# Optimization experiments

Hardware: AMD Instinct MI355X
Metric: run time of the kernel (lower is better)

Reference implementation:

```python
import jax, jax.numpy as jnp
import numpy as np

B, S, D, H = 2, 2048, 1024, 16
HD = D // H  # per-head dim = 64


def setup_inputs() -> dict:
    key = jax.random.key(0)
    ks = jax.random.split(key, 9)
    s = 0.02
    return {
        "h": jax.random.normal(ks[0], (B, S, D), jnp.float32),
        "Wq": jax.random.normal(ks[1], (D, D), jnp.float32) * s,
        "bq": jax.random.normal(ks[2], (D,), jnp.float32) * s,
        "Wk": jax.random.normal(ks[3], (D, D), jnp.float32) * s,
        "bk": jax.random.normal(ks[4], (D,), jnp.float32) * s,
        "Wv": jax.random.normal(ks[5], (D, D), jnp.float32) * s,
        "bv": jax.random.normal(ks[6], (D,), jnp.float32) * s,
        "Wo": jax.random.normal(ks[7], (D, D), jnp.float32) * s,
        "bo": jax.random.normal(ks[8], (D,), jnp.float32) * s,
    }


def reference(h, Wq, bq, Wk, bk, Wv, bv, Wo, bo):
    b, s, d = h.shape
    # Linear projections (torch Linear: x @ W.T + b), split heads -> [B,H,S,HD]
    def split_heads(x):
        return x.reshape(b, s, H, HD).transpose(0, 2, 1, 3)

    q = split_heads(h @ Wq.T + bq)
    k = split_heads(h @ Wk.T + bk)
    v = split_heads(h @ Wv.T + bv)

    # scaled scores [B,H,S,S]
    qk = jnp.einsum("bhqd,bhkd->bhqk", q, k) / np.sqrt(HD).astype(np.float32)
    # causal mask: strictly upper triangle -> -inf
    causal = jnp.triu(jnp.ones((s, s), dtype=bool), k=1)
    qk = jnp.where(causal[None, None], -jnp.inf, qk)

    probs = jax.nn.softmax(qk, axis=-1)
    o = jnp.einsum("bhqk,bhkd->bhqd", probs, v)
    o = o.transpose(0, 2, 1, 3).reshape(b, s, d)
    return o @ Wo.T + bo
```

## Files before the change

### kernel.cpp

```cpp
#include <hip/hip_runtime.h>
#include <stdint.h>

typedef __bf16 bf16;
typedef __bf16 bf16x4_t __attribute__((ext_vector_type(4)));
typedef __bf16 bf16x8_t __attribute__((ext_vector_type(8)));
typedef float f32x4 __attribute__((ext_vector_type(4)));

static constexpr int NB = 2, SS = 2048, DD = 1024, NH = 16, HD = 64;

__device__ __forceinline__ void gl_lds16(const void* g, void* l) {
    __builtin_amdgcn_global_load_lds((__attribute__((address_space(1))) void*)g,
                                     (__attribute__((address_space(3))) void*)l, 16, 0, 0);
}

__global__ __launch_bounds__(256) void cast_all(const float* __restrict__ h,
                                                const float* __restrict__ Wq,
                                                const float* __restrict__ Wk,
                                                const float* __restrict__ Wv,
                                                const float* __restrict__ Wo,
                                                bf16* __restrict__ dst) {
    int i = blockIdx.x * 256 + threadIdx.x;
    const float* src;
    int off;
    if (i < 1048576) { src = h; off = i; }
    else {
        int r = i - 1048576;
        int w = r >> 18;
        off = r & 262143;
        src = (w == 0) ? Wq : (w == 1) ? Wk : (w == 2) ? Wv : Wo;
    }
    float4 v = reinterpret_cast<const float4*>(src)[off];
    bf16x4_t o;
    o.x = (bf16)v.x; o.y = (bf16)v.y; o.z = (bf16)v.z; o.w = (bf16)v.w;
    reinterpret_cast<bf16x4_t*>(dst)[i] = o;
}

__device__ __forceinline__ void gemm128_mainloop(const bf16* __restrict__ Ablk,
                                                 const bf16* __restrict__ Bblk,
                                                 int K, f32x4 acc[4][4]) {
    __shared__ __align__(16) bf16 As[128 * 32];
    __shared__ __align__(16) bf16 Bs[128 * 32];
    const int tid = threadIdx.x;
    const int wave = tid >> 6, lane = tid & 63;
    const int quad = lane >> 4, l15 = lane & 15;
    const int wm = wave >> 1, wn = wave & 1;

#pragma unroll
    for (int mi = 0; mi < 4; mi++)
#pragma unroll
        for (int ni = 0; ni < 4; ni++) {
            acc[mi][ni][0] = 0.f; acc[mi][ni][1] = 0.f;
            acc[mi][ni][2] = 0.f; acc[mi][ni][3] = 0.f;
        }

    const int n0c = tid;
    const int r0 = n0c >> 2, c0 = (n0c & 3) ^ ((r0 >> 1) & 3);
    const int n1c = 256 + tid;
    const int r1 = n1c >> 2, c1 = (n1c & 3) ^ ((r1 >> 1) & 3);

    for (int kk = 0; kk < K; kk += 32) {
        __syncthreads();
        gl_lds16(Ablk + (size_t)r0 * K + kk + c0 * 8, &As[(wave * 64) * 8]);
        gl_lds16(Ablk + (size_t)r1 * K + kk + c1 * 8, &As[(256 + wave * 64) * 8]);
        gl_lds16(Bblk + (size_t)r0 * K + kk + c0 * 8, &Bs[(wave * 64) * 8]);
        gl_lds16(Bblk + (size_t)r1 * K + kk + c1 * 8, &Bs[(256 + wave * 64) * 8]);
        __syncthreads();

        bf16x8_t a[4], b[4];
#pragma unroll
        for (int mi = 0; mi < 4; mi++) {
            int R = wm * 64 + mi * 16 + l15;
            a[mi] = *(const bf16x8_t*)&As[R * 32 + ((quad ^ ((R >> 1) & 3)) << 3)];
        }
#pragma unroll
        for (int ni = 0; ni < 4; ni++) {
            int R = wn * 64 + ni * 16 + l15;
            b[ni] = *(const bf16x8_t*)&Bs[R * 32 + ((quad ^ ((R >> 1) & 3)) << 3)];
        }
#pragma unroll
        for (int mi = 0; mi < 4; mi++)
#pragma unroll
            for (int ni = 0; ni < 4; ni++)
                acc[mi][ni] = __builtin_amdgcn_mfma_f32_16x16x32_bf16(a[mi], b[ni], acc[mi][ni], 0, 0, 0);
    }
}

__device__ __forceinline__ void gemm64_mainloop(const bf16* __restrict__ Ablk,
                                                const bf16* __restrict__ Bblk,
                                                int K, f32x4 acc[2][4]) {
    __shared__ __align__(16) bf16 As[64 * 32];
    __shared__ __align__(16) bf16 Bs[128 * 32];
    const int tid = threadIdx.x;
    const int wave = tid >> 6, lane = tid & 63;
    const int quad = lane >> 4, l15 = lane & 15;
    const int wm = wave >> 1, wn = wave & 1;

#pragma unroll
    for (int mi = 0; mi < 2; mi++)
#pragma unroll
        for (int ni = 0; ni < 4; ni++) {
            acc[mi][ni][0] = 0.f; acc[mi][ni][1] = 0.f;
            acc[mi][ni][2] = 0.f; acc[mi][ni][3] = 0.f;
        }

    const int ra = tid >> 2, ca = (tid & 3) ^ ((ra >> 1) & 3);
    const int r0 = tid >> 2, c0 = (tid & 3) ^ ((r0 >> 1) & 3);
    const int n1c = 256 + tid;
    const int r1 = n1c >> 2, c1 = (n1c & 3) ^ ((r1 >> 1) & 3);

    for (int kk = 0; kk < K; kk += 32) {
        __syncthreads();
        gl_lds16(Ablk + (size_t)ra * K + kk + ca * 8, &As[(wave * 64) * 8]);
        gl_lds16(Bblk + (size_t)r0 * K + kk + c0 * 8, &Bs[(wave * 64) * 8]);
        gl_lds16(Bblk + (size_t)r1 * K + kk + c1 * 8, &Bs[(256 + wave * 64) * 8]);
        __syncthreads();

        bf16x8_t a[2], b[4];
#pragma unroll
        for (int mi = 0; mi < 2; mi++) {
            int R = wm * 32 + mi * 16 + l15;
            a[mi] = *(const bf16x8_t*)&As[R * 32 + ((quad ^ ((R >> 1) & 3)) << 3)];
        }
#pragma unroll
        for (int ni = 0; ni < 4; ni++) {
            int R = wn * 64 + ni * 16 + l15;
            b[ni] = *(const bf16x8_t*)&Bs[R * 32 + ((quad ^ ((R >> 1) & 3)) << 3)];
        }
#pragma unroll
        for (int mi = 0; mi < 2; mi++)
#pragma unroll
            for (int ni = 0; ni < 4; ni++)
                acc[mi][ni] = __builtin_amdgcn_mfma_f32_16x16x32_bf16(a[mi], b[ni], acc[mi][ni], 0, 0, 0);
    }
}

__global__ __launch_bounds__(256) void gemm_qkv(const bf16* __restrict__ A, const bf16* __restrict__ Wqkv,
                                                const float* __restrict__ bq, const float* __restrict__ bk,
                                                const float* __restrict__ bv,
                                                bf16* __restrict__ Qb, bf16* __restrict__ Kb, bf16* __restrict__ Vb) {
    const int m0 = blockIdx.x * 128;
    const int n0 = blockIdx.y * 128;
    f32x4 acc[4][4];
    gemm128_mainloop(A + (size_t)m0 * DD, Wqkv + (size_t)n0 * DD, DD, acc);

    const int tid = threadIdx.x, wave = tid >> 6, lane = tid & 63;
    const int quad = lane >> 4, l15 = lane & 15;
    const int wm = wave >> 1, wn = wave & 1;

    const int which = n0 >> 10;
    const float* bias = (which == 0) ? bq : (which == 1) ? bk : bv;
    bf16* dst = (which == 0) ? Qb : (which == 1) ? Kb : Vb;
    const float sc = (which == 0) ? 0.18033688f : 1.0f;

    const int cbase = (n0 & 1023) + wn * 64;
    const int head = cbase >> 6;
    const int bb = m0 >> 11;
    const int s0 = (m0 & 2047) + wm * 64;
    bf16* dbase = dst + ((size_t)(bb * NH + head)) * SS * HD;

#pragma unroll
    for (int ni = 0; ni < 4; ni++) {
        float bsv = bias[cbase + ni * 16 + l15];
        int hd = ni * 16 + l15;
#pragma unroll
        for (int mi = 0; mi < 4; mi++) {
#pragma unroll
            for (int r = 0; r < 4; r++) {
                int s = s0 + mi * 16 + quad * 4 + r;
                dbase[(size_t)s * HD + hd] = (bf16)((acc[mi][ni][r] + bsv) * sc);
            }
        }
    }
}

__global__ __launch_bounds__(256) void gemm_out(const bf16* __restrict__ A, const bf16* __restrict__ Wo,
                                                const float* __restrict__ bo, float* __restrict__ out) {
    const int m0 = blockIdx.x * 64, n0 = blockIdx.y * 128;
    f32x4 acc[2][4];
    gemm64_mainloop(A + (size_t)m0 * DD, Wo + (size_t)n0 * DD, DD, acc);

    const int tid = threadIdx.x, wave = tid >> 6, lane = tid & 63;
    const int quad = lane >> 4, l15 = lane & 15;
    const int wm = wave >> 1, wn = wave & 1;
    float* obase = out + (size_t)(m0 + wm * 32) * DD + n0 + wn * 64;
#pragma unroll
    for (int ni = 0; ni < 4; ni++) {
        float bias = bo[n0 + wn * 64 + ni * 16 + l15];
#pragma unroll
        for (int mi = 0; mi < 2; mi++)
#pragma unroll
            for (int r = 0; r < 4; r++)
                obase[(size_t)(mi * 16 + quad * 4 + r) * DD + ni * 16 + l15] = acc[mi][ni][r] + bias;
    }
}

__global__ __launch_bounds__(256, 3) void attn_kernel(const bf16* __restrict__ Qb, const bf16* __restrict__ Kb,
                                                      const bf16* __restrict__ Vb, bf16* __restrict__ Ob,
                                                      bf16* __restrict__ Opart, float* __restrict__ Ml) {
    constexpr int PQ[24]  = {15,15,14, 7,14,13,13,12, 6,12,11,11,10, 5,10, 9, 9, 8, 4, 8, 3, 2, 1, 0};
    constexpr int PJ0[24] = { 0, 8, 0, 0, 8, 0, 7, 0, 0, 7, 0, 6, 0, 0, 6, 0, 5, 0, 0, 5, 0, 0, 0, 0};
    constexpr int PJ1[24] = { 8,16, 8, 8,15, 7,14, 7, 7,13, 6,12, 6, 6,11, 5,10, 5, 5, 9, 4, 3, 2, 1};

    __shared__ __align__(16) bf16 Kt[128 * 64];
    __shared__ __align__(16) bf16 Vt[64 * 136];
    __shared__ __align__(16) bf16 Pt[4 * 32 * 64];

    const int tid = threadIdx.x, wave = tid >> 6, lane = tid & 63;
    const int quad = lane >> 4, l15 = lane & 15;
    const int bx = blockIdx.x;
    const int p = bx >> 5, bh = bx & 31;
    const int qtile = PQ[p], jbeg = PJ0[p], jend = PJ1[p];
    const bool diagpart = (jend == qtile + 1);
    const size_t hoff = (size_t)bh * SS * HD;
    const bf16* Qg = Qb + hoff + (size_t)qtile * 128 * HD;

    bf16x8_t qf[2][2];
#pragma unroll
    for (int qt = 0; qt < 2; qt++)
#pragma unroll
        for (int ks = 0; ks < 2; ks++)
            qf[qt][ks] = *(const bf16x8_t*)(Qg + (wave * 32 + qt * 16 + l15) * HD + ks * 32 + quad * 8);

    f32x4 o[2][4];
#pragma unroll
    for (int qt = 0; qt < 2; qt++)
#pragma unroll
        for (int nO = 0; nO < 4; nO++) {
            o[qt][nO][0] = 0.f; o[qt][nO][1] = 0.f; o[qt][nO][2] = 0.f; o[qt][nO][3] = 0.f;
        }
    float mrow[2] = {-__builtin_inff(), -__builtin_inff()};
    float lrow[2] = {0.f, 0.f};

    bf16* Pw = &Pt[wave * 2048];

    for (int j = jbeg; j < jend; j++) {
        __syncthreads();
        const bf16* Kg = Kb + hoff + (size_t)j * 128 * HD;
#pragma unroll
        for (int t = 0; t < 4; t++) {
            int n = t * 256 + tid;
            int row = n >> 3, gc = (n & 7) ^ (row & 7);
            gl_lds16(Kg + row * HD + gc * 8, &Kt[(t * 256 + wave * 64) * 8]);
        }
        const bf16* Vg = Vb + hoff + (size_t)j * 128 * HD;
        {
            int k0 = (tid & 31) * 4, d0 = (tid >> 5) * 8;
            bf16x8_t v0 = *(const bf16x8_t*)(Vg + (k0 + 0) * HD + d0);
            bf16x8_t v1 = *(const bf16x8_t*)(Vg + (k0 + 1) * HD + d0);
            bf16x8_t v2 = *(const bf16x8_t*)(Vg + (k0 + 2) * HD + d0);
            bf16x8_t v3 = *(const bf16x8_t*)(Vg + (k0 + 3) * HD + d0);
#pragma unroll
            for (int jj = 0; jj < 8; jj++) {
                bf16x4_t w;
                w.x = v0[jj]; w.y = v1[jj]; w.z = v2[jj]; w.w = v3[jj];
                *(bf16x4_t*)&Vt[(d0 + jj) * 136 + k0] = w;
            }
        }
        __syncthreads();

        const bool diag = diagpart && (j == jend - 1);
#pragma unroll 1
        for (int kh = 0; kh < 2; kh++) {
            if (diag && kh == 1 && wave < 2) break;

            f32x4 st[4][2];
#pragma unroll
            for (int kt = 0; kt < 4; kt++)
#pragma unroll
                for (int qt = 0; qt < 2; qt++) {
                    st[kt][qt][0] = 0.f; st[kt][qt][1] = 0.f; st[kt][qt][2] = 0.f; st[kt][qt][3] = 0.f;
                }
#pragma unroll
            for (int ks = 0; ks < 2; ks++) {
#pragma unroll
                for (int kt = 0; kt < 4; kt++) {
                    int R = (kh * 4 + kt) * 16 + l15;
                    bf16x8_t kf = *(const bf16x8_t*)&Kt[R * HD + ((((ks << 2) | quad) ^ (R & 7)) << 3)];
#pragma unroll
                    for (int qt = 0; qt < 2; qt++)
                        st[kt][qt] = __builtin_amdgcn_mfma_f32_16x16x32_bf16(kf, qf[qt][ks], st[kt][qt], 0, 0, 0);
                }
            }
            if (diag) {
#pragma unroll
                for (int kt = 0; kt < 4; kt++)
#pragma unroll
                    for (int qt = 0; qt < 2; qt++)
#pragma unroll
                        for (int r = 0; r < 4; r++) {
                            int key = kh * 64 + kt * 16 + quad * 4 + r;
                            int row = wave * 32 + qt * 16 + l15;
                            if (key > row) st[kt][qt][r] = -__builtin_inff();
                        }
            }

#pragma unroll
            for (int qt = 0; qt < 2; qt++) {
                float mx = -__builtin_inff();
#pragma unroll
                for (int kt = 0; kt < 4; kt++)
#pragma unroll
                    for (int r = 0; r < 4; r++) mx = fmaxf(mx, st[kt][qt][r]);
                mx = fmaxf(mx, __shfl_xor(mx, 16));
                mx = fmaxf(mx, __shfl_xor(mx, 32));
                float mnew = fmaxf(mrow[qt], mx);
                float alpha = exp2f(mrow[qt] - mnew);
                mrow[qt] = mnew;
                float sum = 0.f;
                const int row = qt * 16 + l15;
#pragma unroll
                for (int kt = 0; kt < 4; kt++) {
                    float p0 = exp2f(st[kt][qt][0] - mnew);
                    float p1 = exp2f(st[kt][qt][1] - mnew);
                    float p2 = exp2f(st[kt][qt][2] - mnew);
                    float p3 = exp2f(st[kt][qt][3] - mnew);
                    sum += (p0 + p1) + (p2 + p3);
                    bf16x4_t pb;
                    pb.x = (bf16)p0; pb.y = (bf16)p1; pb.z = (bf16)p2; pb.w = (bf16)p3;
                    int c = kt * 2 + (quad >> 1);
                    *(bf16x4_t*)&Pw[row * 64 + ((c ^ (row & 7)) << 3) + ((quad & 1) << 2)] = pb;
                }
                sum += __shfl_xor(sum, 16);
                sum += __shfl_xor(sum, 32);
                lrow[qt] = lrow[qt] * alpha + sum;
#pragma unroll
                for (int r = 0; r < 4; r++) {
                    float a = __shfl(alpha, (lane & 48) | (quad * 4 + r));
#pragma unroll
                    for (int nO = 0; nO < 4; nO++) o[qt][nO][r] *= a;
                }
            }

#pragma unroll
            for (int ks = 0; ks < 2; ks++) {
                bf16x8_t pf[2];
#pragma unroll
                for (int qt = 0; qt < 2; qt++) {
                    int row = qt * 16 + l15;
                    int c = (ks << 2) | quad;
                    pf[qt] = *(const bf16x8_t*)&Pw[row * 64 + ((c ^ (row & 7)) << 3)];
                }
#pragma unroll
                for (int nO = 0; nO < 4; nO++) {
                    bf16x8_t vf = *(const bf16x8_t*)&Vt[(nO * 16 + l15) * 136 + kh * 64 + ks * 32 + quad * 8];
#pragma unroll
                    for (int qt = 0; qt < 2; qt++)
                        o[qt][nO] = __builtin_amdgcn_mfma_f32_16x16x32_bf16(pf[qt], vf, o[qt][nO], 0, 0, 0);
                }
            }
        }
    }

    if (qtile >= 8) {
        const int pidx = ((bh << 3) + (qtile - 8)) * 2 + (jbeg != 0 ? 1 : 0);
        bf16* Op = Opart + (size_t)pidx * (128 * 64);
        float* mlp = Ml + (size_t)pidx * 256;
#pragma unroll
        for (int qt = 0; qt < 2; qt++) {
            if (quad == 0) {
                mlp[wave * 32 + qt * 16 + l15] = mrow[qt];
                mlp[128 + wave * 32 + qt * 16 + l15] = lrow[qt];
            }
#pragma unroll
            for (int r = 0; r < 4; r++) {
                int row = wave * 32 + qt * 16 + quad * 4 + r;
#pragma unroll
                for (int nO = 0; nO < 4; nO++)
                    Op[row * 64 + nO * 16 + l15] = (bf16)o[qt][nO][r];
            }
        }
    } else {
        const int bb = bh >> 4, hh = bh & 15;
#pragma unroll
        for (int qt = 0; qt < 2; qt++) {
#pragma unroll
            for (int r = 0; r < 4; r++) {
                float linv = 1.f / __shfl(lrow[qt], (lane & 48) | (quad * 4 + r));
                int srow = qtile * 128 + wave * 32 + qt * 16 + quad * 4 + r;
#pragma unroll
                for (int nO = 0; nO < 4; nO++)
                    Ob[((size_t)(bb * SS + srow)) * DD + hh * HD + nO * 16 + l15] = (bf16)(o[qt][nO][r] * linv);
            }
        }
    }
}

__global__ __launch_bounds__(256) void merge_kernel(const bf16* __restrict__ Opart,
                                                    const float* __restrict__ Ml,
                                                    bf16* __restrict__ Ob) {
    const int bh = blockIdx.x >> 3, q8 = blockIdx.x & 7;
    const int p0 = ((bh << 3) + q8) * 2, p1 = p0 + 1;
    const int t = threadIdx.x, row = t >> 1, c0 = (t & 1) * 32;
    float m0 = Ml[p0 * 256 + row], l0 = Ml[p0 * 256 + 128 + row];
    float m1 = Ml[p1 * 256 + row], l1 = Ml[p1 * 256 + 128 + row];
    float M = fmaxf(m0, m1);
    float w0 = exp2f(m0 - M), w1 = exp2f(m1 - M);
    float inv = 1.f / (l0 * w0 + l1 * w1);
    w0 *= inv; w1 *= inv;
    const bf16* O0 = Opart + (size_t)p0 * (128 * 64) + row * 64 + c0;
    const bf16* O1 = Opart + (size_t)p1 * (128 * 64) + row * 64 + c0;
    const int bb = bh >> 4, hh = bh & 15;
    const int srow = (8 + q8) * 128 + row;
    bf16* dst = Ob + ((size_t)(bb * SS + srow)) * DD + hh * HD + c0;
#pragma unroll
    for (int i = 0; i < 4; i++) {
        bf16x8_t a = *(const bf16x8_t*)(O0 + i * 8);
        bf16x8_t b = *(const bf16x8_t*)(O1 + i * 8);
        bf16x8_t r;
#pragma unroll
        for (int jj = 0; jj < 8; jj++)
            r[jj] = (bf16)((float)a[jj] * w0 + (float)b[jj] * w1);
        *(bf16x8_t*)(dst + i * 8) = r;
    }
}

extern "C" void kernel_launch(void* const* d_in, const int* in_sizes, int n_in,
                              void* d_out, int out_size, void* d_ws, size_t ws_size,
                              hipStream_t stream) {
    (void)in_sizes; (void)n_in; (void)out_size; (void)ws_size;
    const float* h  = (const float*)d_in[0];
    const float* Wq = (const float*)d_in[1];
    const float* bq = (const float*)d_in[2];
    const float* Wk = (const float*)d_in[3];
    const float* bk = (const float*)d_in[4];
    const float* Wv = (const float*)d_in[5];
    const float* bv = (const float*)d_in[6];
    const float* Wo = (const float*)d_in[7];
    const float* bo = (const float*)d_in[8];
    float* out = (float*)d_out;

    char* ws = (char*)d_ws;
    bf16* hbf  = (bf16*)(ws);
    bf16* wqkv = (bf16*)(ws + 8388608);
    bf16* wo   = (bf16*)(ws + 8388608 + 6291456);
    bf16* Qb   = (bf16*)(ws + 16777216);
    bf16* Kb   = (bf16*)(ws + 16777216 + 8388608);
    bf16* Vb   = (bf16*)(ws + 16777216 + 2 * 8388608);
    bf16* Ob   = (bf16*)(ws + 16777216 + 3 * 8388608);
    bf16*  Opart = (bf16*)(ws);
    float* Ml    = (float*)(ws + 8388608);

    cast_all<<<8192, 256, 0, stream>>>(h, Wq, Wk, Wv, Wo, hbf);
    gemm_qkv<<<dim3(32, 24), 256, 0, stream>>>(hbf, wqkv, bq, bk, bv, Qb, Kb, Vb);
    attn_kernel<<<768, 256, 0, stream>>>(Qb, Kb, Vb, Ob, Opart, Ml);
    merge_kernel<<<256, 256, 0, stream>>>(Opart, Ml, Ob);
    gemm_out<<<dim3(64, 8), 256, 0, stream>>>(Ob, wo, bo, out);
}
```

Baseline: 191.8 us.

## Use atomic work queue for attention tiles and softmax over full 128-key block

Attention blocks now take work items from a global atomic counter, reset by a memset before launch, instead of mapping blockIdx directly to an item. This aims to improve load balance across the unevenly sized causal partitions. Scores for all 128 keys are also computed before a single online-softmax update per K/V tile, replacing two updates of 64 keys each and cutting max/rescale overhead. The costs are a larger score register array, which raises register pressure under the 3-blocks-per-CU bound, losing the diagonal-tile early exit for half the waves, and an extra memset launch.

```diff
diff --git a/kernel.cpp b/kernel.cpp
--- a/kernel.cpp
+++ b/kernel.cpp
@@ -196,7 +196,8 @@
 
 __global__ __launch_bounds__(256, 3) void attn_kernel(const bf16* __restrict__ Qb, const bf16* __restrict__ Kb,
                                                       const bf16* __restrict__ Vb, bf16* __restrict__ Ob,
-                                                      bf16* __restrict__ Opart, float* __restrict__ Ml) {
+                                                      bf16* __restrict__ Opart, float* __restrict__ Ml,
+                                                      int* __restrict__ counter) {
     constexpr int PQ[24]  = {15,15,14, 7,14,13,13,12, 6,12,11,11,10, 5,10, 9, 9, 8, 4, 8, 3, 2, 1, 0};
     constexpr int PJ0[24] = { 0, 8, 0, 0, 8, 0, 7, 0, 0, 7, 0, 6, 0, 0, 6, 0, 5, 0, 0, 5, 0, 0, 0, 0};
     constexpr int PJ1[24] = { 8,16, 8, 8,15, 7,14, 7, 7,13, 6,12, 6, 6,11, 5,10, 5, 5, 9, 4, 3, 2, 1};
@@ -204,68 +205,70 @@
     __shared__ __align__(16) bf16 Kt[128 * 64];
     __shared__ __align__(16) bf16 Vt[64 * 136];
     __shared__ __align__(16) bf16 Pt[4 * 32 * 64];
+    __shared__ int s_item;
 
     const int tid = threadIdx.x, wave = tid >> 6, lane = tid & 63;
     const int quad = lane >> 4, l15 = lane & 15;
-    const int bx = blockIdx.x;
-    const int p = bx >> 5, bh = bx & 31;
-    const int qtile = PQ[p], jbeg = PJ0[p], jend = PJ1[p];
-    const bool diagpart = (jend == qtile + 1);
-    const size_t hoff = (size_t)bh * SS * HD;
-    const bf16* Qg = Qb + hoff + (size_t)qtile * 128 * HD;
-
-    bf16x8_t qf[2][2];
-#pragma unroll
-    for (int qt = 0; qt < 2; qt++)
-#pragma unroll
-        for (int ks = 0; ks < 2; ks++)
-            qf[qt][ks] = *(const bf16x8_t*)(Qg + (wave * 32 + qt * 16 + l15) * HD + ks * 32 + quad * 8);
-
-    f32x4 o[2][4];
-#pragma unroll
-    for (int qt = 0; qt < 2; qt++)
-#pragma unroll
-        for (int nO = 0; nO < 4; nO++) {
-            o[qt][nO][0] = 0.f; o[qt][nO][1] = 0.f; o[qt][nO][2] = 0.f; o[qt][nO][3] = 0.f;
-        }
-    float mrow[2] = {-__builtin_inff(), -__builtin_inff()};
-    float lrow[2] = {0.f, 0.f};
-
     bf16* Pw = &Pt[wave * 2048];
 
-    for (int j = jbeg; j < jend; j++) {
+    for (;;) {
+        if (tid == 0) s_item = atomicAdd(counter, 1);
         __syncthreads();
-        const bf16* Kg = Kb + hoff + (size_t)j * 128 * HD;
-#pragma unroll
-        for (int t = 0; t < 4; t++) {
-            int n = t * 256 + tid;
-            int row = n >> 3, gc = (n & 7) ^ (row & 7);
-            gl_lds16(Kg + row * HD + gc * 8, &Kt[(t * 256 + wave * 64) * 8]);
-        }
-        const bf16* Vg = Vb + hoff + (size_t)j * 128 * HD;
-        {
-            int k0 = (tid & 31) * 4, d0 = (tid >> 5) * 8;
-            bf16x8_t v0 = *(const bf16x8_t*)(Vg + (k0 + 0) * HD + d0);
-            bf16x8_t v1 = *(const bf16x8_t*)(Vg + (k0 + 1) * HD + d0);
-            bf16x8_t v2 = *(const bf16x8_t*)(Vg + (k0 + 2) * HD + d0);
-            bf16x8_t v3 = *(const bf16x8_t*)(Vg + (k0 + 3) * HD + d0);
-#pragma unroll
-            for (int jj = 0; jj < 8; jj++) {
-                bf16x4_t w;
-                w.x = v0[jj]; w.y = v1[jj]; w.z = v2[jj]; w.w = v3[jj];
-                *(bf16x4_t*)&Vt[(d0 + jj) * 136 + k0] = w;
-            }
-        }
-        __syncthreads();
-
-        const bool diag = diagpart && (j == jend - 1);
-#pragma unroll 1
-        for (int kh = 0; kh < 2; kh++) {
-            if (diag && kh == 1 && wave < 2) break;
-
-            f32x4 st[4][2];
-#pragma unroll
-            for (int kt = 0; kt < 4; kt++)
+        const int g = s_item;
+        if (g >= 768) return;
+        const int p = g >> 5, bh = g & 31;
+        const int qtile = PQ[p], jbeg = PJ0[p], jend = PJ1[p];
+        const bool diagpart = (jend == qtile + 1);
+        const size_t hoff = (size_t)bh * SS * HD;
+        const bf16* Qg = Qb + hoff + (size_t)qtile * 128 * HD;
+
+        bf16x8_t qf[2][2];
+#pragma unroll
+        for (int qt = 0; qt < 2; qt++)
+#pragma unroll
+            for (int ks = 0; ks < 2; ks++)
+                qf[qt][ks] = *(const bf16x8_t*)(Qg + (wave * 32 + qt * 16 + l15) * HD + ks * 32 + quad * 8);
+
+        f32x4 o[2][4];
+#pragma unroll
+        for (int qt = 0; qt < 2; qt++)
+#pragma unroll
+            for (int nO = 0; nO < 4; nO++) {
+                o[qt][nO][0] = 0.f; o[qt][nO][1] = 0.f; o[qt][nO][2] = 0.f; o[qt][nO][3] = 0.f;
+            }
+        float mrow[2] = {-__builtin_inff(), -__builtin_inff()};
+        float lrow[2] = {0.f, 0.f};
+
+        for (int j = jbeg; j < jend; j++) {
+            __syncthreads();
+            const bf16* Kg = Kb + hoff + (size_t)j * 128 * HD;
+#pragma unroll
+            for (int t = 0; t < 4; t++) {
+                int n = t * 256 + tid;
+                int row = n >> 3, gc = (n & 7) ^ (row & 7);
+                gl_lds16(Kg + row * HD + gc * 8, &Kt[(t * 256 + wave * 64) * 8]);
+            }
+            const bf16* Vg = Vb + hoff + (size_t)j * 128 * HD;
+            {
+                int k0 = (tid & 31) * 4, d0 = (tid >> 5) * 8;
+                bf16x8_t v0 = *(const bf16x8_t*)(Vg + (k0 + 0) * HD + d0);
+                bf16x8_t v1 = *(const bf16x8_t*)(Vg + (k0 + 1) * HD + d0);
+                bf16x8_t v2 = *(const bf16x8_t*)(Vg + (k0 + 2) * HD + d0);
+                bf16x8_t v3 = *(const bf16x8_t*)(Vg + (k0 + 3) * HD + d0);
+#pragma unroll
+                for (int jj = 0; jj < 8; jj++) {
+                    bf16x4_t w;
+                    w.x = v0[jj]; w.y = v1[jj]; w.z = v2[jj]; w.w = v3[jj];
+                    *(bf16x4_t*)&Vt[(d0 + jj) * 136 + k0] = w;
+                }
+            }
+            __syncthreads();
+
+            const bool diag = diagpart && (j == jend - 1);
+
+            f32x4 st[8][2];
+#pragma unroll
+            for (int kt = 0; kt < 8; kt++)
 #pragma unroll
                 for (int qt = 0; qt < 2; qt++) {
                     st[kt][qt][0] = 0.f; st[kt][qt][1] = 0.f; st[kt][qt][2] = 0.f; st[kt][qt][3] = 0.f;
@@ -273,8 +276,8 @@
 #pragma unroll
             for (int ks = 0; ks < 2; ks++) {
 #pragma unroll
-                for (int kt = 0; kt < 4; kt++) {
-                    int R = (kh * 4 + kt) * 16 + l15;
+                for (int kt = 0; kt < 8; kt++) {
+                    int R = kt * 16 + l15;
                     bf16x8_t kf = *(const bf16x8_t*)&Kt[R * HD + ((((ks << 2) | quad) ^ (R & 7)) << 3)];
 #pragma unroll
                     for (int qt = 0; qt < 2; qt++)
@@ -283,12 +286,12 @@
             }
             if (diag) {
 #pragma unroll
-                for (int kt = 0; kt < 4; kt++)
+                for (int kt = 0; kt < 8; kt++)
 #pragma unroll
                     for (int qt = 0; qt < 2; qt++)
 #pragma unroll
                         for (int r = 0; r < 4; r++) {
-                            int key = kh * 64 + kt * 16 + quad * 4 + r;
+                            int key = kt * 16 + quad * 4 + r;
                             int row = wave * 32 + qt * 16 + l15;
                             if (key > row) st[kt][qt][r] = -__builtin_inff();
                         }
@@ -298,7 +301,7 @@
             for (int qt = 0; qt < 2; qt++) {
                 float mx = -__builtin_inff();
 #pragma unroll
-                for (int kt = 0; kt < 4; kt++)
+                for (int kt = 0; kt < 8; kt++)
 #pragma unroll
                     for (int r = 0; r < 4; r++) mx = fmaxf(mx, st[kt][qt][r]);
                 mx = fmaxf(mx, __shfl_xor(mx, 16));
@@ -307,18 +310,15 @@
                 float alpha = exp2f(mrow[qt] - mnew);
                 mrow[qt] = mnew;
                 float sum = 0.f;
-                const int row = qt * 16 + l15;
-#pragma unroll
-                for (int kt = 0; kt < 4; kt++) {
+#pragma unroll
+                for (int kt = 0; kt < 8; kt++) {
                     float p0 = exp2f(st[kt][qt][0] - mnew);
                     float p1 = exp2f(st[kt][qt][1] - mnew);
                     float p2 = exp2f(st[kt][qt][2] - mnew);
                     float p3 = exp2f(st[kt][qt][3] - mnew);
                     sum += (p0 + p1) + (p2 + p3);
-                    bf16x4_t pb;
-                    pb.x = (bf16)p0; pb.y = (bf16)p1; pb.z = (bf16)p2; pb.w = (bf16)p3;
-                    int c = kt * 2 + (quad >> 1);
-                    *(bf16x4_t*)&Pw[row * 64 + ((c ^ (row & 7)) << 3) + ((quad & 1) << 2)] = pb;
+                    st[kt][qt][0] = p0; st[kt][qt][1] = p1;
+                    st[kt][qt][2] = p2; st[kt][qt][3] = p3;
                 }
                 sum += __shfl_xor(sum, 16);
                 sum += __shfl_xor(sum, 32);
@@ -332,54 +332,70 @@
             }
 
 #pragma unroll
-            for (int ks = 0; ks < 2; ks++) {
-                bf16x8_t pf[2];
+            for (int kh = 0; kh < 2; kh++) {
 #pragma unroll
                 for (int qt = 0; qt < 2; qt++) {
-                    int row = qt * 16 + l15;
-                    int c = (ks << 2) | quad;
-                    pf[qt] = *(const bf16x8_t*)&Pw[row * 64 + ((c ^ (row & 7)) << 3)];
-                }
-#pragma unroll
-                for (int nO = 0; nO < 4; nO++) {
-                    bf16x8_t vf = *(const bf16x8_t*)&Vt[(nO * 16 + l15) * 136 + kh * 64 + ks * 32 + quad * 8];
-#pragma unroll
-                    for (int qt = 0; qt < 2; qt++)
-                        o[qt][nO] = __builtin_amdgcn_mfma_f32_16x16x32_bf16(pf[qt], vf, o[qt][nO], 0, 0, 0);
-                }
-            }
-        }
-    }
-
-    if (qtile >= 8) {
-        const int pidx = ((bh << 3) + (qtile - 8)) * 2 + (jbeg != 0 ? 1 : 0);
-        bf16* Op = Opart + (size_t)pidx * (128 * 64);
-        float* mlp = Ml + (size_t)pidx * 256;
-#pragma unroll
-        for (int qt = 0; qt < 2; qt++) {
-            if (quad == 0) {
-                mlp[wave * 32 + qt * 16 + l15] = mrow[qt];
-                mlp[128 + wave * 32 + qt * 16 + l15] = lrow[qt];
-            }
-#pragma unroll
-            for (int r = 0; r < 4; r++) {
-                int row = wave * 32 + qt * 16 + quad * 4 + r;
-#pragma unroll
-                for (int nO = 0; nO < 4; nO++)
-                    Op[row * 64 + nO * 16 + l15] = (bf16)o[qt][nO][r];
-            }
-        }
-    } else {
-        const int bb = bh >> 4, hh = bh & 15;
-#pragma unroll
-        for (int qt = 0; qt < 2; qt++) {
-#pragma unroll
-            for (int r = 0; r < 4; r++) {
-                float linv = 1.f / __shfl(lrow[qt], (lane & 48) | (quad * 4 + r));
-                int srow = qtile * 128 + wave * 32 + qt * 16 + quad * 4 + r;
-#pragma unroll
-                for (int nO = 0; nO < 4; nO++)
-                    Ob[((size_t)(bb * SS + srow)) * DD + hh * HD + nO * 16 + l15] = (bf16)(o[qt][nO][r] * linv);
+                    const int row = qt * 16 + l15;
+#pragma unroll
+                    for (int kt4 = 0; kt4 < 4; kt4++) {
+                        const int kt = kh * 4 + kt4;
+                        bf16x4_t pb;
+                        pb.x = (bf16)st[kt][qt][0]; pb.y = (bf16)st[kt][qt][1];
+                        pb.z = (bf16)st[kt][qt][2]; pb.w = (bf16)st[kt][qt][3];
+                        int c = kt4 * 2 + (quad >> 1);
+                        *(bf16x4_t*)&Pw[row * 64 + ((c ^ (row & 7)) << 3) + ((quad & 1) << 2)] = pb;
+                    }
+                }
+#pragma unroll
+                for (int ks = 0; ks < 2; ks++) {
+                    bf16x8_t pf[2];
+#pragma unroll
+                    for (int qt = 0; qt < 2; qt++) {
+                        int row = qt * 16 + l15;
+                        int c = (ks << 2) | quad;
+                        pf[qt] = *(const bf16x8_t*)&Pw[row * 64 + ((c ^ (row & 7)) << 3)];
+                    }
+#pragma unroll
+                    for (int nO = 0; nO < 4; nO++) {
+                        bf16x8_t vf = *(const bf16x8_t*)&Vt[(nO * 16 + l15) * 136 + kh * 64 + ks * 32 + quad * 8];
+#pragma unroll
+                        for (int qt = 0; qt < 2; qt++)
+                            o[qt][nO] = __builtin_amdgcn_mfma_f32_16x16x32_bf16(pf[qt], vf, o[qt][nO], 0, 0, 0);
+                    }
+                }
+            }
+        }
+
+        if (qtile >= 8) {
+            const int pidx = ((bh << 3) + (qtile - 8)) * 2 + (jbeg != 0 ? 1 : 0);
+            bf16* Op = Opart + (size_t)pidx * (128 * 64);
+            float* mlp = Ml + (size_t)pidx * 256;
+#pragma unroll
+            for (int qt = 0; qt < 2; qt++) {
+                if (quad == 0) {
+                    mlp[wave * 32 + qt * 16 + l15] = mrow[qt];
+                    mlp[128 + wave * 32 + qt * 16 + l15] = lrow[qt];
+                }
+#pragma unroll
+                for (int r = 0; r < 4; r++) {
+                    int row = wave * 32 + qt * 16 + quad * 4 + r;
+#pragma unroll
+                    for (int nO = 0; nO < 4; nO++)
+                        Op[row * 64 + nO * 16 + l15] = (bf16)o[qt][nO][r];
+                }
+            }
+        } else {
+            const int bb = bh >> 4, hh = bh & 15;
+#pragma unroll
+            for (int qt = 0; qt < 2; qt++) {
+#pragma unroll
+                for (int r = 0; r < 4; r++) {
+                    float linv = 1.f / __shfl(lrow[qt], (lane & 48) | (quad * 4 + r));
+                    int srow = qtile * 128 + wave * 32 + qt * 16 + quad * 4 + r;
+#pragma unroll
+                    for (int nO = 0; nO < 4; nO++)
+                        Ob[((size_t)(bb * SS + srow)) * DD + hh * HD + nO * 16 + l15] = (bf16)(o[qt][nO][r] * linv);
+                }
             }
         }
     }
@@ -437,12 +453,14 @@
     bf16* Kb   = (bf16*)(ws + 16777216 + 8388608);
     bf16* Vb   = (bf16*)(ws + 16777216 + 2 * 8388608);
     bf16* Ob   = (bf16*)(ws + 16777216 + 3 * 8388608);
-    bf16*  Opart = (bf16*)(ws);
-    float* Ml    = (float*)(ws + 8388608);
+    bf16*  Opart   = (bf16*)(ws);
+    float* Ml      = (float*)(ws + 8388608);
+    int*   counter = (int*)(ws + 8912896);
 
     cast_all<<<8192, 256, 0, stream>>>(h, Wq, Wk, Wv, Wo, hbf);
     gemm_qkv<<<dim3(32, 24), 256, 0, stream>>>(hbf, wqkv, bq, bk, bv, Qb, Kb, Vb);
-    attn_kernel<<<768, 256, 0, stream>>>(Qb, Kb, Vb, Ob, Opart, Ml);
+    hipMemsetAsync(counter, 0, 4, stream);
+    attn_kernel<<<768, 256, 0, stream>>>(Qb, Kb, Vb, Ob, Opart, Ml, counter);
     merge_kernel<<<256, 256, 0, stream>>>(Opart, Ml, Ob);
     gemm_out<<<dim3(64, 8), 256, 0, stream>>>(Ob, wo, bo, out);
 }
```

Result: slower. 225.1 us (+17.3%).

## Fuse split-KV merge into attention kernel via atomic completion flags

Applied to the files above, without the earlier changes.

Removes the separate merge kernel: each split-KV half writes its partial output and max/sum stats, then bumps an atomic counter per tile pair. The second finisher reads the other half's partial and writes the combined normalized output directly. The work-item schedule table is also reordered. This saves one launch and the partial-buffer round trip for the merged half, at the cost of a memset launch, fences and a serialized tail inside the attention blocks.

```diff
diff --git a/kernel.cpp b/kernel.cpp
--- a/kernel.cpp
+++ b/kernel.cpp
@@ -196,14 +196,16 @@
 
 __global__ __launch_bounds__(256, 3) void attn_kernel(const bf16* __restrict__ Qb, const bf16* __restrict__ Kb,
                                                       const bf16* __restrict__ Vb, bf16* __restrict__ Ob,
-                                                      bf16* __restrict__ Opart, float* __restrict__ Ml) {
-    constexpr int PQ[24]  = {15,15,14, 7,14,13,13,12, 6,12,11,11,10, 5,10, 9, 9, 8, 4, 8, 3, 2, 1, 0};
-    constexpr int PJ0[24] = { 0, 8, 0, 0, 8, 0, 7, 0, 0, 7, 0, 6, 0, 0, 6, 0, 5, 0, 0, 5, 0, 0, 0, 0};
-    constexpr int PJ1[24] = { 8,16, 8, 8,15, 7,14, 7, 7,13, 6,12, 6, 6,11, 5,10, 5, 5, 9, 4, 3, 2, 1};
+                                                      bf16* __restrict__ Opart, float* __restrict__ Ml,
+                                                      int* __restrict__ flags) {
+    constexpr int PQ[24]  = {15,15,14,14,13,13,12,12,  7, 6,11,11,10,10, 9, 5,  0, 1, 2, 3, 8, 9, 8, 4};
+    constexpr int PJ0[24] = { 0, 8, 0, 8, 0, 7, 0, 7,  0, 0, 0, 6, 0, 6, 0, 0,  0, 0, 0, 0, 5, 5, 0, 0};
+    constexpr int PJ1[24] = { 8,16, 8,15, 7,14, 7,13,  8, 7, 6,12, 6,11, 5, 6,  1, 2, 3, 4, 9,10, 5, 5};
 
     __shared__ __align__(16) bf16 Kt[128 * 64];
     __shared__ __align__(16) bf16 Vt[64 * 136];
     __shared__ __align__(16) bf16 Pt[4 * 32 * 64];
+    __shared__ int s_old;
 
     const int tid = threadIdx.x, wave = tid >> 6, lane = tid & 63;
     const int quad = lane >> 4, l15 = lane & 15;
@@ -213,6 +215,7 @@
     const bool diagpart = (jend == qtile + 1);
     const size_t hoff = (size_t)bh * SS * HD;
     const bf16* Qg = Qb + hoff + (size_t)qtile * 128 * HD;
+    bf16* Pw = &Pt[wave * 2048];
 
     bf16x8_t qf[2][2];
 #pragma unroll
@@ -230,8 +233,6 @@
         }
     float mrow[2] = {-__builtin_inff(), -__builtin_inff()};
     float lrow[2] = {0.f, 0.f};
-
-    bf16* Pw = &Pt[wave * 2048];
 
     for (int j = jbeg; j < jend; j++) {
         __syncthreads();
@@ -351,8 +352,11 @@
         }
     }
 
+    const int bb = bh >> 4, hh = bh & 15;
     if (qtile >= 8) {
-        const int pidx = ((bh << 3) + (qtile - 8)) * 2 + (jbeg != 0 ? 1 : 0);
+        const int pairidx = (bh << 3) + (qtile - 8);
+        const int half = (jbeg != 0) ? 1 : 0;
+        const int pidx = pairidx * 2 + half;
         bf16* Op = Opart + (size_t)pidx * (128 * 64);
         float* mlp = Ml + (size_t)pidx * 256;
 #pragma unroll
@@ -369,8 +373,38 @@
                     Op[row * 64 + nO * 16 + l15] = (bf16)o[qt][nO][r];
             }
         }
+        __threadfence();
+        __syncthreads();
+        if (tid == 0) s_old = atomicAdd(&flags[pairidx], 1);
+        __syncthreads();
+        if (s_old == 1) {
+            __threadfence();
+            const int pother = pidx ^ 1;
+            const bf16* Oo = Opart + (size_t)pother * (128 * 64);
+            const float* mlo = Ml + (size_t)pother * 256;
+#pragma unroll
+            for (int qt = 0; qt < 2; qt++) {
+#pragma unroll
+                for (int r = 0; r < 4; r++) {
+                    int row = wave * 32 + qt * 16 + quad * 4 + r;
+                    float m_own = __shfl(mrow[qt], (lane & 48) | (quad * 4 + r));
+                    float l_own = __shfl(lrow[qt], (lane & 48) | (quad * 4 + r));
+                    float m_p = mlo[row];
+                    float l_p = mlo[128 + row];
+                    float M = fmaxf(m_own, m_p);
+                    float w_own = exp2f(m_own - M), w_p = exp2f(m_p - M);
+                    float inv = 1.f / (l_own * w_own + l_p * w_p);
+                    int srow = qtile * 128 + row;
+#pragma unroll
+                    for (int nO = 0; nO < 4; nO++) {
+                        float vp = (float)Oo[row * 64 + nO * 16 + l15];
+                        float v = (o[qt][nO][r] * w_own + vp * w_p) * inv;
+                        Ob[((size_t)(bb * SS + srow)) * DD + hh * HD + nO * 16 + l15] = (bf16)v;
+                    }
+                }
+            }
+        }
     } else {
-        const int bb = bh >> 4, hh = bh & 15;
 #pragma unroll
         for (int qt = 0; qt < 2; qt++) {
 #pragma unroll
@@ -382,35 +416,6 @@
                     Ob[((size_t)(bb * SS + srow)) * DD + hh * HD + nO * 16 + l15] = (bf16)(o[qt][nO][r] * linv);
             }
         }
-    }
-}
-
-__global__ __launch_bounds__(256) void merge_kernel(const bf16* __restrict__ Opart,
-                                                    const float* __restrict__ Ml,
-                                                    bf16* __restrict__ Ob) {
-    const int bh = blockIdx.x >> 3, q8 = blockIdx.x & 7;
-    const int p0 = ((bh << 3) + q8) * 2, p1 = p0 + 1;
-    const int t = threadIdx.x, row = t >> 1, c0 = (t & 1) * 32;
-    float m0 = Ml[p0 * 256 + row], l0 = Ml[p0 * 256 + 128 + row];
-    float m1 = Ml[p1 * 256 + row], l1 = Ml[p1 * 256 + 128 + row];
-    float M = fmaxf(m0, m1);
-    float w0 = exp2f(m0 - M), w1 = exp2f(m1 - M);
-    float inv = 1.f / (l0 * w0 + l1 * w1);
-    w0 *= inv; w1 *= inv;
-    const bf16* O0 = Opart + (size_t)p0 * (128 * 64) + row * 64 + c0;
-    const bf16* O1 = Opart + (size_t)p1 * (128 * 64) + row * 64 + c0;
-    const int bb = bh >> 4, hh = bh & 15;
-    const int srow = (8 + q8) * 128 + row;
-    bf16* dst = Ob + ((size_t)(bb * SS + srow)) * DD + hh * HD + c0;
-#pragma unroll
-    for (int i = 0; i < 4; i++) {
-        bf16x8_t a = *(const bf16x8_t*)(O0 + i * 8);
-        bf16x8_t b = *(const bf16x8_t*)(O1 + i * 8);
-        bf16x8_t r;
-#pragma unroll
-        for (int jj = 0; jj < 8; jj++)
-            r[jj] = (bf16)((float)a[jj] * w0 + (float)b[jj] * w1);
-        *(bf16x8_t*)(dst + i * 8) = r;
     }
 }
 
@@ -439,10 +444,11 @@
     bf16* Ob   = (bf16*)(ws + 16777216 + 3 * 8388608);
     bf16*  Opart = (bf16*)(ws);
     float* Ml    = (float*)(ws + 8388608);
+    int*   flags = (int*)(ws + 8912896);
 
     cast_all<<<8192, 256, 0, stream>>>(h, Wq, Wk, Wv, Wo, hbf);
     gemm_qkv<<<dim3(32, 24), 256, 0, stream>>>(hbf, wqkv, bq, bk, bv, Qb, Kb, Vb);
-    attn_kernel<<<768, 256, 0, stream>>>(Qb, Kb, Vb, Ob, Opart, Ml);
-    merge_kernel<<<256, 256, 0, stream>>>(Opart, Ml, Ob);
+    hipMemsetAsync(flags, 0, 1024, stream);
+    attn_kernel<<<768, 256, 0, stream>>>(Qb, Kb, Vb, Ob, Opart, Ml, flags);
     gemm_out<<<dim3(64, 8), 256, 0, stream>>>(Ob, wo, bo, out);
 }
```

Result: slower. 283.0 us (+47.5%).

## Store V transposed from QKV GEMM and load it into LDS asynchronously

Applied to the files above, without the earlier changes.

The QKV projection epilogue now writes V in a head-dim-major (transposed) layout with vectorized 4-element stores. The attention kernel can then copy V tiles straight into LDS with direct global-to-LDS loads and an XOR swizzle, replacing the register-level transpose and padded LDS layout. The attention block schedule is also reordered so the longest work items are dispatched first. In exchange, the GEMM epilogue writes V with a larger stride, and the swizzled V reads must avoid LDS bank conflicts without padding.

```diff
diff --git a/kernel.cpp b/kernel.cpp
--- a/kernel.cpp
+++ b/kernel.cpp
@@ -149,25 +149,44 @@
 
     const int which = n0 >> 10;
     const float* bias = (which == 0) ? bq : (which == 1) ? bk : bv;
-    bf16* dst = (which == 0) ? Qb : (which == 1) ? Kb : Vb;
     const float sc = (which == 0) ? 0.18033688f : 1.0f;
 
     const int cbase = (n0 & 1023) + wn * 64;
     const int head = cbase >> 6;
     const int bb = m0 >> 11;
     const int s0 = (m0 & 2047) + wm * 64;
-    bf16* dbase = dst + ((size_t)(bb * NH + head)) * SS * HD;
-
-#pragma unroll
-    for (int ni = 0; ni < 4; ni++) {
-        float bsv = bias[cbase + ni * 16 + l15];
-        int hd = ni * 16 + l15;
-#pragma unroll
-        for (int mi = 0; mi < 4; mi++) {
-#pragma unroll
-            for (int r = 0; r < 4; r++) {
-                int s = s0 + mi * 16 + quad * 4 + r;
-                dbase[(size_t)s * HD + hd] = (bf16)((acc[mi][ni][r] + bsv) * sc);
+
+    if (which == 2) {
+        bf16* dbase = Vb + ((size_t)(bb * NH + head)) * HD * SS;
+#pragma unroll
+        for (int ni = 0; ni < 4; ni++) {
+            float bsv = bias[cbase + ni * 16 + l15];
+            int hd = ni * 16 + l15;
+#pragma unroll
+            for (int mi = 0; mi < 4; mi++) {
+                bf16x4_t pb;
+                pb.x = (bf16)(acc[mi][ni][0] + bsv);
+                pb.y = (bf16)(acc[mi][ni][1] + bsv);
+                pb.z = (bf16)(acc[mi][ni][2] + bsv);
+                pb.w = (bf16)(acc[mi][ni][3] + bsv);
+                int s = s0 + mi * 16 + quad * 4;
+                *(bf16x4_t*)&dbase[(size_t)hd * SS + s] = pb;
+            }
+        }
+    } else {
+        bf16* dst = (which == 0) ? Qb : Kb;
+        bf16* dbase = dst + ((size_t)(bb * NH + head)) * SS * HD;
+#pragma unroll
+        for (int ni = 0; ni < 4; ni++) {
+            float bsv = bias[cbase + ni * 16 + l15];
+            int hd = ni * 16 + l15;
+#pragma unroll
+            for (int mi = 0; mi < 4; mi++) {
+#pragma unroll
+                for (int r = 0; r < 4; r++) {
+                    int s = s0 + mi * 16 + quad * 4 + r;
+                    dbase[(size_t)s * HD + hd] = (bf16)((acc[mi][ni][r] + bsv) * sc);
+                }
             }
         }
     }
@@ -197,12 +216,12 @@
 __global__ __launch_bounds__(256, 3) void attn_kernel(const bf16* __restrict__ Qb, const bf16* __restrict__ Kb,
                                                       const bf16* __restrict__ Vb, bf16* __restrict__ Ob,
                                                       bf16* __restrict__ Opart, float* __restrict__ Ml) {
-    constexpr int PQ[24]  = {15,15,14, 7,14,13,13,12, 6,12,11,11,10, 5,10, 9, 9, 8, 4, 8, 3, 2, 1, 0};
-    constexpr int PJ0[24] = { 0, 8, 0, 0, 8, 0, 7, 0, 0, 7, 0, 6, 0, 0, 6, 0, 5, 0, 0, 5, 0, 0, 0, 0};
-    constexpr int PJ1[24] = { 8,16, 8, 8,15, 7,14, 7, 7,13, 6,12, 6, 6,11, 5,10, 5, 5, 9, 4, 3, 2, 1};
+    constexpr int PQ[24]  = {15,14,13,12,11,10, 9, 8, 15, 7, 14, 6, 13, 5, 12, 4, 11, 3, 10, 2,  9, 1,  8, 0};
+    constexpr int PJ0[24] = { 0, 0, 0, 0, 0, 0, 0, 0,  8, 0,  8, 0,  8, 0,  8, 0,  8, 0,  8, 0,  8, 0,  8, 0};
+    constexpr int PJ1[24] = { 8, 8, 8, 8, 8, 8, 8, 8, 16, 8, 15, 7, 14, 6, 13, 5, 12, 4, 11, 3, 10, 2,  9, 1};
 
     __shared__ __align__(16) bf16 Kt[128 * 64];
-    __shared__ __align__(16) bf16 Vt[64 * 136];
+    __shared__ __align__(16) bf16 Vt[64 * 128];
     __shared__ __align__(16) bf16 Pt[4 * 32 * 64];
 
     const int tid = threadIdx.x, wave = tid >> 6, lane = tid & 63;
@@ -213,6 +232,8 @@
     const bool diagpart = (jend == qtile + 1);
     const size_t hoff = (size_t)bh * SS * HD;
     const bf16* Qg = Qb + hoff + (size_t)qtile * 128 * HD;
+    const bf16* Vbase = Vb + (size_t)bh * HD * SS;
+    bf16* Pw = &Pt[wave * 2048];
 
     bf16x8_t qf[2][2];
 #pragma unroll
@@ -230,8 +251,6 @@
         }
     float mrow[2] = {-__builtin_inff(), -__builtin_inff()};
     float lrow[2] = {0.f, 0.f};
-
-    bf16* Pw = &Pt[wave * 2048];
 
     for (int j = jbeg; j < jend; j++) {
         __syncthreads();
@@ -242,19 +261,12 @@
             int row = n >> 3, gc = (n & 7) ^ (row & 7);
             gl_lds16(Kg + row * HD + gc * 8, &Kt[(t * 256 + wave * 64) * 8]);
         }
-        const bf16* Vg = Vb + hoff + (size_t)j * 128 * HD;
-        {
-            int k0 = (tid & 31) * 4, d0 = (tid >> 5) * 8;
-            bf16x8_t v0 = *(const bf16x8_t*)(Vg + (k0 + 0) * HD + d0);
-            bf16x8_t v1 = *(const bf16x8_t*)(Vg + (k0 + 1) * HD + d0);
-            bf16x8_t v2 = *(const bf16x8_t*)(Vg + (k0 + 2) * HD + d0);
-            bf16x8_t v3 = *(const bf16x8_t*)(Vg + (k0 + 3) * HD + d0);
-#pragma unroll
-            for (int jj = 0; jj < 8; jj++) {
-                bf16x4_t w;
-                w.x = v0[jj]; w.y = v1[jj]; w.z = v2[jj]; w.w = v3[jj];
-                *(bf16x4_t*)&Vt[(d0 + jj) * 136 + k0] = w;
-            }
+        const bf16* Vg = Vbase + j * 128;
+#pragma unroll
+        for (int t = 0; t < 4; t++) {
+            int n = t * 256 + tid;
+            int row = n >> 4, gc = (n & 15) ^ (row & 15);
+            gl_lds16(Vg + (size_t)row * SS + gc * 8, &Vt[(t * 256 + wave * 64) * 8]);
         }
         __syncthreads();
 
@@ -342,7 +354,8 @@
                 }
 #pragma unroll
                 for (int nO = 0; nO < 4; nO++) {
-                    bf16x8_t vf = *(const bf16x8_t*)&Vt[(nO * 16 + l15) * 136 + kh * 64 + ks * 32 + quad * 8];
+                    int c = kh * 8 + ks * 4 + quad;
+                    bf16x8_t vf = *(const bf16x8_t*)&Vt[(nO * 16 + l15) * 128 + ((c ^ l15) << 3)];
 #pragma unroll
                     for (int qt = 0; qt < 2; qt++)
                         o[qt][nO] = __builtin_amdgcn_mfma_f32_16x16x32_bf16(pf[qt], vf, o[qt][nO], 0, 0, 0);
@@ -351,6 +364,7 @@
         }
     }
 
+    const int bb = bh >> 4, hh = bh & 15;
     if (qtile >= 8) {
         const int pidx = ((bh << 3) + (qtile - 8)) * 2 + (jbeg != 0 ? 1 : 0);
         bf16* Op = Opart + (size_t)pidx * (128 * 64);
@@ -370,7 +384,6 @@
             }
         }
     } else {
-        const int bb = bh >> 4, hh = bh & 15;
 #pragma unroll
         for (int qt = 0; qt < 2; qt++) {
 #pragma unroll
```

Measured after the change: 187.9 us. 2.0% less time.
